# Performance work log

Measured on AMD Instinct MI355X. Metric: run time of the kernel, lower is better.

Reference implementation:

```python
import jax, jax.numpy as jnp
import numpy as np

N_NODES = 100000
N_EDGES = 500000
N_GRAPHS = 128
HID = 128          # Config.hidden_dim
KEY_EMB = HID // 4 # 32
IN_DIM = 16
FEAT_DIM = IN_DIM - 1  # key feature removed
OUT_DIM = 2
MSG_IN = 2 * HID + 1   # 257


def setup_inputs() -> dict:
    key = jax.random.key(0)
    ks = jax.random.split(key, 24)
    p = lambda k, shp: (jax.random.normal(k, shp, dtype=jnp.float32) * 0.02)
    inp = {
        "x": jax.random.normal(ks[0], (N_NODES, IN_DIM), dtype=jnp.float32),
        "W_enc": p(ks[1], (1, KEY_EMB)), "b_enc": jnp.zeros((KEY_EMB,), jnp.float32),
        "W0": p(ks[2], (FEAT_DIM + KEY_EMB, HID)), "b0": jnp.zeros((HID,), jnp.float32),
        "W1a": p(ks[3], (MSG_IN, HID)), "b1a": jnp.zeros((HID,), jnp.float32),
        "W1b": p(ks[4], (HID, HID)), "b1b": jnp.zeros((HID,), jnp.float32),
        "W2a": p(ks[5], (MSG_IN, HID)), "b2a": jnp.zeros((HID,), jnp.float32),
        "W2b": p(ks[6], (HID, HID)), "b2b": jnp.zeros((HID,), jnp.float32),
        "Wf1": p(ks[7], (4 * HID, HID)), "bf1": jnp.zeros((HID,), jnp.float32),
        "Wf2": p(ks[8], (HID, OUT_DIM)), "bf2": jnp.zeros((OUT_DIM,), jnp.float32),
        "edge_src1": jax.random.randint(ks[9], (N_EDGES,), 0, N_NODES),
        "edge_dst1": jax.random.randint(ks[10], (N_EDGES,), 0, N_NODES),
        "edge_src2": jax.random.randint(ks[11], (N_EDGES,), 0, N_NODES),
        "edge_dst2": jax.random.randint(ks[12], (N_EDGES,), 0, N_NODES),
        "batch": jnp.sort(jax.random.randint(ks[13], (N_NODES,), 0, N_GRAPHS)),
    }
    return inp


def _leaky_relu(v):
    return jnp.where(v > 0, v, 0.1 * v)


def _edge_conv(h, key_feat, src, dst, Wa, ba, Wb, bb):
    # message: [x_j - x_i, x_i, key_j - key_i] -> Linear -> LeakyReLU(0.1) -> Linear
    h_i = h[dst]                      # [E, HID] target
    h_j = h[src]                      # [E, HID] source
    m = jnp.concatenate([h_j - h_i, h_i, key_feat[src] - key_feat[dst]], axis=-1)  # [E, 257]
    m = _leaky_relu(jnp.dot(m, Wa) + ba)
    m = jnp.dot(m, Wb) + bb
    agg = jax.ops.segment_max(m, dst, num_segments=N_NODES)
    agg = jnp.where(jnp.isfinite(agg), agg, 0.0)  # nodes with no in-edges -> 0 (PyG scatter-max fill)
    return agg + h  # residual


def reference(x, W_enc, b_enc, W0, b0, W1a, b1a, W1b, b1b, W2a, b2a, W2b, b2b,
              Wf1, bf1, Wf2, bf2, edge_src1, edge_dst1, edge_src2, edge_dst2, batch):
    key_feat = x[:, 0:1]              # key_feature_idx = 0
    features = x[:, 1:]               # [N, FEAT_DIM]
    key_emb = jnp.dot(key_feat, W_enc) + b_enc  # [N, 32]
    h = jax.nn.relu(jnp.dot(jnp.concatenate([features, key_emb], axis=-1), W0) + b0)  # dropout: eval mode

    x1 = jax.nn.relu(_edge_conv(h, key_feat, edge_src1, edge_dst1, W1a, b1a, W1b, b1b))
    x2 = jax.nn.relu(_edge_conv(x1, key_feat, edge_src2, edge_dst2, W2a, b2a, W2b, b2b))

    cat = jnp.concatenate([x1, x2], axis=1)  # [N, 256]
    max_pool = jax.ops.segment_max(cat, batch, num_segments=N_GRAPHS)
    max_pool = jnp.where(jnp.isfinite(max_pool), max_pool, 0.0)
    counts = jax.ops.segment_sum(jnp.ones((N_NODES,), jnp.float32), batch, num_segments=N_GRAPHS)
    mean_pool = jax.ops.segment_sum(cat, batch, num_segments=N_GRAPHS) / jnp.maximum(counts, 1.0)[:, None]

    pooled = jnp.concatenate([max_pool, mean_pool], axis=1)  # [G, 512]
    out = jnp.dot(jax.nn.relu(jnp.dot(pooled, Wf1) + bf1), Wf2) + bf2
    return jax.nn.log_softmax(out, axis=1)
```

## Files before the change

### kernel.cpp

```cpp
#include <hip/hip_runtime.h>
#include <cstdint>

#define N_NODES 100000
#define N_EDGES 500000
#define N_GRAPHS 128
#define HID 128
#define SCAN1_B ((2 * N_NODES + 255) / 256)
#define BOTH_GRID ((2 * N_EDGES + 255) / 256)
#define MM_G ((N_NODES + 127) / 128)
#define A_G ((2 * N_NODES + 511) / 512)
#define B_G ((2 * N_EDGES + 511) / 512)

typedef __attribute__((ext_vector_type(8))) short short8;
typedef __attribute__((ext_vector_type(4))) float f32x4;

__device__ __forceinline__ unsigned encf(float f) {
    unsigned u = __float_as_uint(f);
    return (u & 0x80000000u) ? ~u : (u | 0x80000000u);
}
__device__ __forceinline__ float decf(unsigned e) {
    unsigned u = (e & 0x80000000u) ? (e & 0x7FFFFFFFu) : ~e;
    return __uint_as_float(u);
}
__device__ __forceinline__ unsigned cvt_pk_bf16(float lo, float hi) {
    unsigned r;
    asm("v_cvt_pk_bf16_f32 %0, %1, %2" : "=v"(r) : "v"(lo), "v"(hi));
    return r;
}
__device__ __forceinline__ ushort bf16r(float f) {
    unsigned u = __float_as_uint(f);
    return (ushort)((u + 0x7fffu + ((u >> 16) & 1u)) >> 16);
}
__device__ __forceinline__ float bf2f(ushort h) {
    return __uint_as_float((unsigned)h << 16);
}

__global__ __launch_bounds__(256) void prep_hist_kernel(const float* __restrict__ W1b,
                                                        const float* __restrict__ W2b,
                                                        const float* __restrict__ W1a,
                                                        const float* __restrict__ W2a,
                                                        const float* __restrict__ W_enc,
                                                        const float* __restrict__ b_enc,
                                                        const float* __restrict__ W0,
                                                        const float* __restrict__ b0,
                                                        ushort* __restrict__ WT,
                                                        float* __restrict__ wkey,
                                                        float* __restrict__ bias0,
                                                        float* __restrict__ pooled,
                                                        const int* __restrict__ dst1,
                                                        const int* __restrict__ dst2,
                                                        int* __restrict__ cnt,
                                                        int* __restrict__ seq) {
    int blk = blockIdx.x;
    int tid = threadIdx.x;
    if (blk >= 641) {
        int e = (blk - 641) * 256 + tid;
        if (e < N_EDGES) seq[e] = atomicAdd(&cnt[dst1[e]], 1);
        else if (e < 2 * N_EDGES) seq[e] = atomicAdd(&cnt[N_NODES + dst2[e - N_EDGES]], 1);
        return;
    }
    if (blk >= 385) {
        pooled[(blk - 385) * 256 + tid] = 0.f;
        return;
    }
    if (blk == 384) {
        if (tid < HID) {
            float wk = 0.f, bk = b0[tid];
            for (int k = 0; k < 32; ++k) {
                float w = W0[(15 + k) * HID + tid];
                wk += W_enc[k] * w;
                bk += b_enc[k] * w;
            }
            wkey[tid] = wk;
            bias0[tid] = bk;
        }
        return;
    }
    int m = blk >> 6;
    int i = (blk & 63) * 256 + tid;
    int n = i >> 7, k = i & 127;
    int src = k * HID + n;
    float v;
    switch (m) {
        case 0: v = W1b[src]; break;
        case 1: v = W2b[src]; break;
        case 2: v = W1a[src]; break;
        case 3: v = W1a[HID * HID + src] - W1a[src]; break;
        case 4: v = W2a[src]; break;
        default: v = W2a[HID * HID + src] - W2a[src]; break;
    }
    WT[m * HID * HID + i] = bf16r(v);
}

__global__ __launch_bounds__(256) void scan1_kernel(const int* __restrict__ cnt,
                                                    int* __restrict__ cursor,
                                                    int* __restrict__ partials) {
    __shared__ int tmp[256];
    int tid = threadIdx.x;
    int gid = blockIdx.x * 256 + tid;
    int v = (gid < 2 * N_NODES) ? cnt[gid] : 0;
    tmp[tid] = v;
    __syncthreads();
#pragma unroll
    for (int off = 1; off < 256; off <<= 1) {
        int t = (tid >= off) ? tmp[tid - off] : 0;
        __syncthreads();
        tmp[tid] += t;
        __syncthreads();
    }
    if (gid < 2 * N_NODES) cursor[gid] = tmp[tid] - v;
    if (tid == 255) partials[blockIdx.x] = tmp[255];
}

__global__ __launch_bounds__(1024) void scan2_kernel(int* __restrict__ partials) {
    __shared__ int tmp[1024];
    int tid = threadIdx.x;
    int v = (tid < SCAN1_B) ? partials[tid] : 0;
    tmp[tid] = v;
    __syncthreads();
#pragma unroll
    for (int off = 1; off < 1024; off <<= 1) {
        int t = (tid >= off) ? tmp[tid - off] : 0;
        __syncthreads();
        tmp[tid] += t;
        __syncthreads();
    }
    if (tid < SCAN1_B) partials[tid] = tmp[tid] - v;
}

__global__ __launch_bounds__(512, 4) void build_mm_kernel(const float* __restrict__ x,
                                                          const float* __restrict__ W0,
                                                          const float* __restrict__ wkey,
                                                          const float* __restrict__ bias0,
                                                          ushort* __restrict__ h,
                                                          float* __restrict__ xkey,
                                                          const ushort* __restrict__ WuT,
                                                          const ushort* __restrict__ WvT,
                                                          const float* __restrict__ bv,
                                                          ushort* __restrict__ outu,
                                                          ushort* __restrict__ outv,
                                                          const int* __restrict__ src1,
                                                          const int* __restrict__ dst1,
                                                          const int* __restrict__ src2,
                                                          const int* __restrict__ dst2,
                                                          const int* __restrict__ cnt,
                                                          const int* __restrict__ cursor,
                                                          const int* __restrict__ partials,
                                                          const int* __restrict__ seq,
                                                          int* __restrict__ srcS,
                                                          int* __restrict__ dstS,
                                                          unsigned* __restrict__ agg1,
                                                          unsigned* __restrict__ agg2) {
    __shared__ ushort sH[128 * 136];
    __shared__ ushort sWT[128 * 136];
    int blk = blockIdx.x;
    int tid = threadIdx.x;

    if (blk >= MM_G) {
        int zb = blk - MM_G;
        if (zb < A_G) {
            int gid = zb * 512 + tid;
            if (gid >= 2 * N_NODES) return;
            int c = cnt[gid];
            if (c == 0) return;
            int o = cursor[gid] + partials[gid >> 8];
            int layer = gid >= N_NODES;
            int d = gid - layer * N_NODES;
            for (int i = 0; i < c; ++i) dstS[o + i] = d;
            bool spans = (o >> 4) != ((o + c - 1) >> 4);
            bool tail = (o + c == N_EDGES) || (o + c == 2 * N_EDGES);
            if (spans || tail) {
                unsigned* agg = layer ? agg2 : agg1;
                uint4* ap = (uint4*)(agg + (size_t)d * HID);
#pragma unroll
                for (int i = 0; i < 32; ++i) ap[i] = make_uint4(0u, 0u, 0u, 0u);
            }
            return;
        }
        int e = (zb - A_G) * 512 + tid;
        int s, idx;
        if (e < N_EDGES) { s = src1[e]; idx = dst1[e]; }
        else if (e < 2 * N_EDGES) { s = src2[e - N_EDGES]; idx = N_NODES + dst2[e - N_EDGES]; }
        else return;
        int pos = cursor[idx] + partials[idx >> 8] + seq[e];
        srcS[pos] = s;
        return;
    }

    int n0 = blk * 128;
#pragma unroll
    for (int q = 0; q < 4; ++q) {
        int c = q * 512 + tid;
        int r = c >> 4, off = (c & 15) << 3;
        int n = n0 + r;
        uint4 vv = make_uint4(0, 0, 0, 0);
        if (n < N_NODES) {
            const float* xr = x + n * 16;
            float k0 = xr[0];
            if (off == 0) xkey[n] = k0;
            float xf[15];
#pragma unroll
            for (int f = 0; f < 15; ++f) xf[f] = xr[1 + f];
            unsigned ow[4];
#pragma unroll
            for (int p = 0; p < 4; ++p) {
                int c0 = off + 2 * p;
                float a0 = bias0[c0] + k0 * wkey[c0];
                float a1 = bias0[c0 + 1] + k0 * wkey[c0 + 1];
#pragma unroll
                for (int f = 0; f < 15; ++f) {
                    float2 w2 = *(const float2*)(W0 + f * HID + c0);
                    a0 = fmaf(xf[f], w2.x, a0);
                    a1 = fmaf(xf[f], w2.y, a1);
                }
                ow[p] = cvt_pk_bf16(fmaxf(a0, 0.f), fmaxf(a1, 0.f));
            }
            vv = make_uint4(ow[0], ow[1], ow[2], ow[3]);
            *(uint4*)(h + (size_t)n * HID + off) = vv;
        }
        *(uint4*)(sH + r * 136 + off) = vv;
    }
#pragma unroll
    for (int q = 0; q < 4; ++q) {
        int c = q * 512 + tid;
        int nn = c >> 4, off = (c & 15) << 3;
        *(uint4*)(sWT + nn * 136 + off) = *(const uint4*)(WuT + nn * 128 + off);
    }
    __syncthreads();

    int lane = tid & 63, wv = tid >> 6;
    int l15 = lane & 15, quad = lane >> 4;
    int ch = wv & 1, rh = wv >> 1;

    short8 afr[2][4];
#pragma unroll
    for (int rr = 0; rr < 2; ++rr) {
        const ushort* ab = sH + (rh * 32 + rr * 16 + l15) * 136 + quad * 8;
#pragma unroll
        for (int kc = 0; kc < 4; ++kc)
            afr[rr][kc] = *(const short8*)(ab + kc * 32);
    }

#pragma unroll
    for (int pass = 0; pass < 2; ++pass) {
        ushort* out = pass ? outv : outu;
        f32x4 acc[2][4];
#pragma unroll
        for (int rr = 0; rr < 2; ++rr)
#pragma unroll
            for (int ct = 0; ct < 4; ++ct) acc[rr][ct] = (f32x4){0.f, 0.f, 0.f, 0.f};
#pragma unroll
        for (int kc = 0; kc < 4; ++kc) {
#pragma unroll
            for (int ct = 0; ct < 4; ++ct) {
                short8 bfr = *(const short8*)(sWT + ((ch * 4 + ct) * 16 + l15) * 136 + quad * 8 + kc * 32);
                acc[0][ct] = __builtin_amdgcn_mfma_f32_16x16x32_bf16(afr[0][kc], bfr, acc[0][ct], 0, 0, 0);
                acc[1][ct] = __builtin_amdgcn_mfma_f32_16x16x32_bf16(afr[1][kc], bfr, acc[1][ct], 0, 0, 0);
            }
        }
        __syncthreads();
#pragma unroll
        for (int ct = 0; ct < 4; ++ct) {
            int col = (ch * 4 + ct) * 16 + l15;
            float bb = pass ? bv[col] : 0.f;
#pragma unroll
            for (int rr = 0; rr < 2; ++rr) {
                int rowb = rh * 32 + rr * 16 + quad * 4;
                unsigned p01 = cvt_pk_bf16(acc[rr][ct][0] + bb, acc[rr][ct][1] + bb);
                unsigned p23 = cvt_pk_bf16(acc[rr][ct][2] + bb, acc[rr][ct][3] + bb);
                sH[(rowb + 0) * 136 + col] = (ushort)p01;
                sH[(rowb + 1) * 136 + col] = (ushort)(p01 >> 16);
                sH[(rowb + 2) * 136 + col] = (ushort)p23;
                sH[(rowb + 3) * 136 + col] = (ushort)(p23 >> 16);
            }
        }
        if (pass == 0) {
#pragma unroll
            for (int q = 0; q < 4; ++q) {
                int c = q * 512 + tid;
                int nn = c >> 4, off = (c & 15) << 3;
                *(uint4*)(sWT + nn * 136 + off) = *(const uint4*)(WvT + nn * 128 + off);
            }
        }
        __syncthreads();
#pragma unroll
        for (int q = 0; q < 4; ++q) {
            int c = q * 512 + tid;
            int r = c >> 4, off = (c & 15) << 3;
            int m = n0 + r;
            if (m < N_NODES)
                *(uint4*)(out + (size_t)m * HID + off) = *(const uint4*)(sH + r * 136 + off);
        }
    }
}

__global__ __launch_bounds__(512, 4) void mm_mfma_dual_kernel(const ushort* __restrict__ in,
                                                              const unsigned* __restrict__ aggin,
                                                              const int* __restrict__ cntin,
                                                              const float* __restrict__ baddin,
                                                              ushort* __restrict__ xout,
                                                              const ushort* __restrict__ WuT,
                                                              const ushort* __restrict__ WvT,
                                                              const float* __restrict__ bv,
                                                              ushort* __restrict__ outu,
                                                              ushort* __restrict__ outv, int nrows) {
    __shared__ ushort sH[128 * 136];
    __shared__ ushort sWT[128 * 136];
    int tid = threadIdx.x;
    int n0 = blockIdx.x * 128;
#pragma unroll
    for (int q = 0; q < 4; ++q) {
        int c = q * 512 + tid;
        int r = c >> 4, off = (c & 15) << 3;
        int n = n0 + r;
        uint4 vv = make_uint4(0, 0, 0, 0);
        if (n < nrows) {
            uint4 hv = *(const uint4*)(in + (size_t)n * HID + off);
            float add[8];
#pragma unroll
            for (int p = 0; p < 8; ++p) add[p] = 0.f;
            if (cntin[n] > 0) {
                uint4 e0 = *(const uint4*)(aggin + (size_t)n * HID + off);
                uint4 e1 = *(const uint4*)(aggin + (size_t)n * HID + off + 4);
                float4 bb0 = *(const float4*)(baddin + off);
                float4 bb1 = *(const float4*)(baddin + off + 4);
                add[0] = decf(e0.x) + bb0.x; add[1] = decf(e0.y) + bb0.y;
                add[2] = decf(e0.z) + bb0.z; add[3] = decf(e0.w) + bb0.w;
                add[4] = decf(e1.x) + bb1.x; add[5] = decf(e1.y) + bb1.y;
                add[6] = decf(e1.z) + bb1.z; add[7] = decf(e1.w) + bb1.w;
            }
            unsigned hw[4] = {hv.x, hv.y, hv.z, hv.w};
            unsigned ow[4];
#pragma unroll
            for (int p = 0; p < 4; ++p) {
                float lo = __uint_as_float(hw[p] << 16);
                float hi = __uint_as_float(hw[p] & 0xffff0000u);
                float r0 = fmaxf(add[2 * p] + lo, 0.f);
                float r1 = fmaxf(add[2 * p + 1] + hi, 0.f);
                ow[p] = cvt_pk_bf16(r0, r1);
            }
            vv = make_uint4(ow[0], ow[1], ow[2], ow[3]);
            *(uint4*)(xout + (size_t)n * HID + off) = vv;
        }
        *(uint4*)(sH + r * 136 + off) = vv;
    }
#pragma unroll
    for (int q = 0; q < 4; ++q) {
        int c = q * 512 + tid;
        int nn = c >> 4, off = (c & 15) << 3;
        *(uint4*)(sWT + nn * 136 + off) = *(const uint4*)(WuT + nn * 128 + off);
    }
    __syncthreads();

    int lane = tid & 63, wv = tid >> 6;
    int l15 = lane & 15, quad = lane >> 4;
    int ch = wv & 1, rh = wv >> 1;

    short8 afr[2][4];
#pragma unroll
    for (int rr = 0; rr < 2; ++rr) {
        const ushort* ab = sH + (rh * 32 + rr * 16 + l15) * 136 + quad * 8;
#pragma unroll
        for (int kc = 0; kc < 4; ++kc)
            afr[rr][kc] = *(const short8*)(ab + kc * 32);
    }

#pragma unroll
    for (int pass = 0; pass < 2; ++pass) {
        ushort* out = pass ? outv : outu;
        f32x4 acc[2][4];
#pragma unroll
        for (int rr = 0; rr < 2; ++rr)
#pragma unroll
            for (int ct = 0; ct < 4; ++ct) acc[rr][ct] = (f32x4){0.f, 0.f, 0.f, 0.f};
#pragma unroll
        for (int kc = 0; kc < 4; ++kc) {
#pragma unroll
            for (int ct = 0; ct < 4; ++ct) {
                short8 bfr = *(const short8*)(sWT + ((ch * 4 + ct) * 16 + l15) * 136 + quad * 8 + kc * 32);
                acc[0][ct] = __builtin_amdgcn_mfma_f32_16x16x32_bf16(afr[0][kc], bfr, acc[0][ct], 0, 0, 0);
                acc[1][ct] = __builtin_amdgcn_mfma_f32_16x16x32_bf16(afr[1][kc], bfr, acc[1][ct], 0, 0, 0);
            }
        }
        __syncthreads();
#pragma unroll
        for (int ct = 0; ct < 4; ++ct) {
            int col = (ch * 4 + ct) * 16 + l15;
            float bb = pass ? bv[col] : 0.f;
#pragma unroll
            for (int rr = 0; rr < 2; ++rr) {
                int rowb = rh * 32 + rr * 16 + quad * 4;
                unsigned p01 = cvt_pk_bf16(acc[rr][ct][0] + bb, acc[rr][ct][1] + bb);
                unsigned p23 = cvt_pk_bf16(acc[rr][ct][2] + bb, acc[rr][ct][3] + bb);
                sH[(rowb + 0) * 136 + col] = (ushort)p01;
                sH[(rowb + 1) * 136 + col] = (ushort)(p01 >> 16);
                sH[(rowb + 2) * 136 + col] = (ushort)p23;
                sH[(rowb + 3) * 136 + col] = (ushort)(p23 >> 16);
            }
        }
        if (pass == 0) {
#pragma unroll
            for (int q = 0; q < 4; ++q) {
                int c = q * 512 + tid;
                int nn = c >> 4, off = (c & 15) << 3;
                *(uint4*)(sWT + nn * 136 + off) = *(const uint4*)(WvT + nn * 128 + off);
            }
        }
        __syncthreads();
#pragma unroll
        for (int q = 0; q < 4; ++q) {
            int c = q * 512 + tid;
            int r = c >> 4, off = (c & 15) << 3;
            int m = n0 + r;
            if (m < nrows)
                *(uint4*)(out + (size_t)m * HID + off) = *(const uint4*)(sH + r * 136 + off);
        }
    }
}

__global__ __launch_bounds__(512, 6) void edge_kernel(const ushort* __restrict__ u,
                                                      const ushort* __restrict__ v,
                                                      const float* __restrict__ xkey,
                                                      const int* __restrict__ srcS,
                                                      const int* __restrict__ dstS,
                                                      const ushort* __restrict__ WbT,
                                                      const float* __restrict__ wlast,
                                                      unsigned* __restrict__ agg) {
    __shared__ ushort sWT[128 * 136];
    __shared__ ushort sU[64 * 136];
    __shared__ int sDst[64];
    __shared__ int sBnd[2];
    __shared__ unsigned sMask[3];
    int tid = threadIdx.x;

    int nwg = gridDim.x;
    int orig = blockIdx.x;
    int qq = nwg >> 3, rr8 = nwg & 7;
    int xcd = orig & 7, idx = orig >> 3;
    int wgid = (xcd < rr8 ? xcd * (qq + 1) : rr8 * (qq + 1) + (xcd - rr8) * qq) + idx;
    int w0 = wgid * 64;

#pragma unroll
    for (int q = 0; q < 4; ++q) {
        int c = q * 512 + tid;
        int n = c >> 4, off = (c & 15) << 3;
        *(uint4*)(sWT + n * 136 + off) = *(const uint4*)(WbT + n * 128 + off);
    }

    int eloc = tid >> 3;
    int sub = tid & 7;
    int kb = sub << 4;
    int lane = tid & 63, wv = tid >> 6;
    int l15 = lane & 15, quad = lane >> 4;
    int ch = wv & 1, rh = wv >> 1;

    float wreg[16];
    {
        const float4* wr4 = (const float4*)(wlast + kb);
#pragma unroll
        for (int q = 0; q < 4; ++q) {
            float4 wq = wr4[q];
            wreg[q * 4 + 0] = wq.x; wreg[q * 4 + 1] = wq.y;
            wreg[q * 4 + 2] = wq.z; wreg[q * 4 + 3] = wq.w;
        }
    }

    {
        int e = w0 + eloc;
        if (e >= N_EDGES) e = N_EDGES - 1;
        int sx = srcS[e], sy = dstS[e];
        if (sub == 0) sDst[eloc] = sy;
        if (tid < 2) {
            int eb = (tid == 0) ? (w0 - 1) : (w0 + 64);
            sBnd[tid] = (eb >= 0 && eb < N_EDGES) ? dstS[eb] : -1;
        }
        float kd = xkey[sx] - xkey[sy];
        const uint4* ur = (const uint4*)(u + (size_t)sx * HID + kb);
        const uint4* vr = (const uint4*)(v + (size_t)sy * HID + kb);
        uint4 uu[2], vvv[2];
        uu[0] = ur[0]; uu[1] = ur[1];
        vvv[0] = vr[0]; vvv[1] = vr[1];
#pragma unroll
        for (int q = 0; q < 2; ++q) {
            unsigned pu[4] = {uu[q].x, uu[q].y, uu[q].z, uu[q].w};
            unsigned pv[4] = {vvv[q].x, vvv[q].y, vvv[q].z, vvv[q].w};
            unsigned pk[4];
#pragma unroll
            for (int p = 0; p < 4; ++p) {
                float a0 = __uint_as_float(pu[p] << 16) + __uint_as_float(pv[p] << 16);
                float a1 = __uint_as_float(pu[p] & 0xffff0000u) + __uint_as_float(pv[p] & 0xffff0000u);
                a0 = fmaf(kd, wreg[q * 8 + 2 * p], a0);
                a1 = fmaf(kd, wreg[q * 8 + 2 * p + 1], a1);
                a0 = fmaxf(a0, 0.1f * a0);
                a1 = fmaxf(a1, 0.1f * a1);
                pk[p] = cvt_pk_bf16(a0, a1);
            }
            uint4 o; o.x = pk[0]; o.y = pk[1]; o.z = pk[2]; o.w = pk[3];
            *(uint4*)(sU + eloc * 136 + kb + q * 8) = o;
        }
    }
    __syncthreads();

    if (tid < 64) {
        int dprev = (tid == 0) ? sBnd[0] : sDst[tid - 1];
        unsigned long long m = __ballot(sDst[tid] != dprev);
        if (tid == 0) { sMask[0] = (unsigned)m; sMask[1] = (unsigned)(m >> 32); }
        if (tid == 63) sMask[2] = (sDst[63] != sBnd[1]) ? 1u : 0u;
    }

    short8 afr[4];
    {
        const ushort* ab = sU + (rh * 16 + l15) * 136 + quad * 8;
#pragma unroll
        for (int kc = 0; kc < 4; ++kc)
            afr[kc] = *(const short8*)(ab + kc * 32);
    }
    f32x4 acc[4];
#pragma unroll
    for (int ct = 0; ct < 4; ++ct) acc[ct] = (f32x4){0.f, 0.f, 0.f, 0.f};
#pragma unroll
    for (int kc = 0; kc < 4; ++kc) {
#pragma unroll
        for (int ct = 0; ct < 4; ++ct) {
            short8 bfr = *(const short8*)(sWT + ((ch * 4 + ct) * 16 + l15) * 136 + quad * 8 + kc * 32);
            acc[ct] = __builtin_amdgcn_mfma_f32_16x16x32_bf16(afr[kc], bfr, acc[ct], 0, 0, 0);
        }
    }
    __syncthreads();

#pragma unroll
    for (int ct = 0; ct < 4; ++ct) {
        int col = (ch * 4 + ct) * 16 + l15;
        uint2 pr;
        pr.x = cvt_pk_bf16(acc[ct][0], acc[ct][1]);
        pr.y = cvt_pk_bf16(acc[ct][2], acc[ct][3]);
        *(uint2*)(sU + col * 66 + rh * 16 + quad * 4) = pr;
    }
    __syncthreads();

    {
        int j = tid & 127;
        int q4 = tid >> 7;
        int base = q4 * 16;
        const ushort* mrow = sU + j * 66 + base;
        float vals[16];
#pragma unroll
        for (int q = 0; q < 4; ++q) {
            ushort4 mv = *(const ushort4*)(mrow + q * 4);
            vals[q * 4 + 0] = bf2f(mv.x);
            vals[q * 4 + 1] = bf2f(mv.y);
            vals[q * 4 + 2] = bf2f(mv.z);
            vals[q * 4 + 3] = bf2f(mv.w);
        }
        unsigned mlo = __builtin_amdgcn_readfirstlane(sMask[0]);
        unsigned mhi = __builtin_amdgcn_readfirstlane(sMask[1]);
        unsigned b64 = __builtin_amdgcn_readfirstlane(sMask[2]);
        unsigned long long mask = ((unsigned long long)mhi << 32) | mlo;
        unsigned slice = (unsigned)((mask >> base) & 0xFFFFull);
        unsigned nextbit = (q4 == 3) ? (b64 & 1u) : (unsigned)((mask >> (base + 16)) & 1ull);
        unsigned ext = slice | (nextbit << 16);
        bool contFrom = !(ext & 1u);
        float run = 0.f;
        bool first = true;
#pragma unroll
        for (int e3 = 0; e3 < 16; ++e3) {
            float vv2 = vals[e3];
            bool hb = (ext >> e3) & 1u;
            run = (e3 == 0 || hb) ? vv2 : fmaxf(run, vv2);
            bool end = (e3 == 15) || ((ext >> (e3 + 1)) & 1u);
            if (end) {
                int d = sDst[base + e3];
                unsigned en = encf(run);
                unsigned* ap = agg + (size_t)d * HID + j;
                bool useAtomic = (first && contFrom) || ((e3 == 15) && !nextbit);
                if (useAtomic) atomicMax(ap, en);
                else *ap = en;
                first = false;
            }
        }
    }
}

__global__ __launch_bounds__(256) void pool_kernel(const ushort* __restrict__ x1,
                                                   const unsigned* __restrict__ agg2,
                                                   const float* __restrict__ b2b,
                                                   const int* __restrict__ cnt2,
                                                   const int* __restrict__ batch,
                                                   float* __restrict__ pooled) {
    int g = blockIdx.x >> 4, s = blockIdx.x & 15;
    int tid = threadIdx.x;
    int lo = 0, hi = N_NODES;
    while (lo < hi) { int mid = (lo + hi) >> 1; if (batch[mid] < g) lo = mid + 1; else hi = mid; }
    int start = lo;
    hi = N_NODES;
    while (lo < hi) { int mid = (lo + hi) >> 1; if (batch[mid] < g + 1) lo = mid + 1; else hi = mid; }
    int end = lo;
    int cnt = end - start;
    int b0 = start + (int)((long long)cnt * s / 16);
    int b1 = start + (int)((long long)cnt * (s + 1) / 16);
    if (b1 <= b0) return;
    int j = tid & 127;
    bool isx2 = tid >= 128;
    float bbj = isx2 ? b2b[j] : 0.f;
    float mx = -INFINITY, sm = 0.f;
    for (int n = b0; n < b1; ++n) {
        float xv = bf2f(x1[(size_t)n * HID + j]);
        float vv;
        if (isx2) {
            float a = 0.f;
            if (cnt2[n] > 0) a = decf(agg2[(size_t)n * HID + j]) + bbj;
            vv = fmaxf(a + xv, 0.f);
        } else {
            vv = xv;
        }
        mx = fmaxf(mx, vv);
        sm += vv;
    }
    atomicMax((unsigned*)pooled + (size_t)g * 512 + tid, encf(mx));
    atomicAdd(pooled + (size_t)g * 512 + 256 + tid, sm);
}

__global__ __launch_bounds__(128) void final_kernel(const float* __restrict__ pooled,
                                                    const int* __restrict__ batch,
                                                    const float* __restrict__ Wf1,
                                                    const float* __restrict__ bf1,
                                                    const float* __restrict__ Wf2,
                                                    const float* __restrict__ bf2,
                                                    float* __restrict__ out) {
    __shared__ float sP[512];
    __shared__ float sH[128];
    int g = blockIdx.x, tid = threadIdx.x;
    int lo = 0, hi = N_NODES;
    while (lo < hi) { int mid = (lo + hi) >> 1; if (batch[mid] < g) lo = mid + 1; else hi = mid; }
    int start = lo;
    hi = N_NODES;
    while (lo < hi) { int mid = (lo + hi) >> 1; if (batch[mid] < g + 1) lo = mid + 1; else hi = mid; }
    int cnt = lo - start;
    float inv = 1.f / (float)(cnt > 1 ? cnt : 1);
#pragma unroll
    for (int q = 0; q < 4; ++q) {
        int idx = q * 128 + tid;
        float raw;
        if (idx < 256) {
            unsigned e = ((const unsigned*)pooled)[(size_t)g * 512 + idx];
            raw = (e == 0u) ? 0.f : decf(e);
        } else {
            raw = pooled[(size_t)g * 512 + idx] * inv;
        }
        sP[idx] = raw;
    }
    __syncthreads();
    float acc = bf1[tid];
    for (int k = 0; k < 512; ++k) acc = fmaf(sP[k], Wf1[k * HID + tid], acc);
    sH[tid] = fmaxf(acc, 0.f);
    __syncthreads();
    if (tid < 2) {
        float l = bf2[tid];
        for (int k = 0; k < 128; ++k) l = fmaf(sH[k], Wf2[k * 2 + tid], l);
        sP[tid] = l;
    }
    __syncthreads();
    if (tid == 0) {
        float l0 = sP[0], l1 = sP[1];
        float m = fmaxf(l0, l1);
        float ls = m + logf(expf(l0 - m) + expf(l1 - m));
        out[g * 2 + 0] = l0 - ls;
        out[g * 2 + 1] = l1 - ls;
    }
}

extern "C" void kernel_launch(void* const* d_in, const int* in_sizes, int n_in,
                              void* d_out, int out_size, void* d_ws, size_t ws_size,
                              hipStream_t stream) {
    const float* x     = (const float*)d_in[0];
    const float* W_enc = (const float*)d_in[1];
    const float* b_enc = (const float*)d_in[2];
    const float* W0    = (const float*)d_in[3];
    const float* b0    = (const float*)d_in[4];
    const float* W1a   = (const float*)d_in[5];
    const float* b1a   = (const float*)d_in[6];
    const float* W1b   = (const float*)d_in[7];
    const float* b1b   = (const float*)d_in[8];
    const float* W2a   = (const float*)d_in[9];
    const float* b2a   = (const float*)d_in[10];
    const float* W2b   = (const float*)d_in[11];
    const float* b2b   = (const float*)d_in[12];
    const float* Wf1   = (const float*)d_in[13];
    const float* bf1   = (const float*)d_in[14];
    const float* Wf2   = (const float*)d_in[15];
    const float* bf2   = (const float*)d_in[16];
    const int* src1    = (const int*)d_in[17];
    const int* dst1    = (const int*)d_in[18];
    const int* src2    = (const int*)d_in[19];
    const int* dst2    = (const int*)d_in[20];
    const int* batch   = (const int*)d_in[21];

    const size_t NB = (size_t)N_NODES * HID;
    ushort* hbuf  = (ushort*)d_ws;
    unsigned* agg1 = (unsigned*)(hbuf + NB);
    unsigned* agg2 = agg1 + NB;
    ushort* ubuf  = (ushort*)(agg2 + NB);
    ushort* vbuf  = ubuf + NB;
    ushort* WT    = vbuf + NB;
    ushort* WbT1 = WT;
    ushort* WbT2 = WT + 1 * HID * HID;
    ushort* WuT1 = WT + 2 * HID * HID;
    ushort* WvT1 = WT + 3 * HID * HID;
    ushort* WuT2 = WT + 4 * HID * HID;
    ushort* WvT2 = WT + 5 * HID * HID;
    float* wkey  = (float*)(WT + 6 * HID * HID);
    float* bias0 = wkey + 128;
    float* xkey  = bias0 + 128;
    float* pooled = xkey + N_NODES;
    int* cnt    = (int*)(pooled + 128 * 512);
    int* cursor = cnt + 2 * N_NODES;
    int* partials = cursor + 2 * N_NODES;
    int* srcS = partials + 1024;
    int* dstS = srcS + 2 * N_EDGES;
    int* seq  = dstS + 2 * N_EDGES;

    const int edgeGrid = (N_EDGES + 63) / 64;
    const int prepGrid = 385 + 256 + BOTH_GRID;
    const int buildMmGrid = MM_G + A_G + B_G;

    hipMemsetAsync(cnt, 0, 2 * N_NODES * sizeof(int), stream);
    prep_hist_kernel<<<prepGrid, 256, 0, stream>>>(W1b, W2b, W1a, W2a, W_enc, b_enc, W0, b0,
                                                   WT, wkey, bias0, pooled, dst1, dst2, cnt, seq);
    scan1_kernel<<<SCAN1_B, 256, 0, stream>>>(cnt, cursor, partials);
    scan2_kernel<<<1, 1024, 0, stream>>>(partials);

    build_mm_kernel<<<buildMmGrid, 512, 0, stream>>>(x, W0, wkey, bias0, hbuf, xkey,
                                                     WuT1, WvT1, b1a, ubuf, vbuf,
                                                     src1, dst1, src2, dst2, cnt, cursor,
                                                     partials, seq, srcS, dstS, agg1, agg2);

    edge_kernel<<<edgeGrid, 512, 0, stream>>>(ubuf, vbuf, xkey, srcS, dstS, WbT1,
                                              W1a + 256 * HID, agg1);

    mm_mfma_dual_kernel<<<MM_G, 512, 0, stream>>>(hbuf, agg1, cnt, b1b, hbuf,
                                                  WuT2, WvT2, b2a, ubuf, vbuf, N_NODES);
    edge_kernel<<<edgeGrid, 512, 0, stream>>>(ubuf, vbuf, xkey, srcS + N_EDGES, dstS + N_EDGES,
                                              WbT2, W2a + 256 * HID, agg2);

    pool_kernel<<<N_GRAPHS * 16, 256, 0, stream>>>(hbuf, agg2, b2b, cnt + N_NODES, batch, pooled);
    final_kernel<<<N_GRAPHS, 128, 0, stream>>>(pooled, batch, Wf1, bf1, Wf2, bf2, (float*)d_out);
}
```

Before: 441.9 us.

## Split layer-2 CSR build across later kernels to shorten the critical path

The layer-2 edge histogram, scan and scatter move out of the up-front prep and build kernels. The histogram now runs inside build_mm_kernel, the scans run after it, and the scatter is fused into the layer-2 node matmul kernel as extra blocks. The aim is to shrink the serial prep phase and hide the layer-2 CSR work behind useful matmul work. It adds two more small scan launches and extra grid blocks in mm2.

```diff
diff --git a/kernel.cpp b/kernel.cpp
--- a/kernel.cpp
+++ b/kernel.cpp
@@ -5,11 +5,11 @@
 #define N_EDGES 500000
 #define N_GRAPHS 128
 #define HID 128
-#define SCAN1_B ((2 * N_NODES + 255) / 256)
-#define BOTH_GRID ((2 * N_EDGES + 255) / 256)
+#define SCANH_B ((N_NODES + 255) / 256)
+#define E256_G ((N_EDGES + 255) / 256)
 #define MM_G ((N_NODES + 127) / 128)
-#define A_G ((2 * N_NODES + 511) / 512)
-#define B_G ((2 * N_EDGES + 511) / 512)
+#define AH_G ((N_NODES + 511) / 512)
+#define BH_G ((N_EDGES + 511) / 512)
 
 typedef __attribute__((ext_vector_type(8))) short short8;
 typedef __attribute__((ext_vector_type(4))) float f32x4;
@@ -48,7 +48,6 @@
                                                         float* __restrict__ bias0,
                                                         float* __restrict__ pooled,
                                                         const int* __restrict__ dst1,
-                                                        const int* __restrict__ dst2,
                                                         int* __restrict__ cnt,
                                                         int* __restrict__ seq) {
     int blk = blockIdx.x;
@@ -56,7 +55,6 @@
     if (blk >= 641) {
         int e = (blk - 641) * 256 + tid;
         if (e < N_EDGES) seq[e] = atomicAdd(&cnt[dst1[e]], 1);
-        else if (e < 2 * N_EDGES) seq[e] = atomicAdd(&cnt[N_NODES + dst2[e - N_EDGES]], 1);
         return;
     }
     if (blk >= 385) {
@@ -92,13 +90,13 @@
     WT[m * HID * HID + i] = bf16r(v);
 }
 
-__global__ __launch_bounds__(256) void scan1_kernel(const int* __restrict__ cnt,
-                                                    int* __restrict__ cursor,
-                                                    int* __restrict__ partials) {
+__global__ __launch_bounds__(256) void scan_half_kernel(const int* __restrict__ cnt,
+                                                        int* __restrict__ cursor,
+                                                        int* __restrict__ partials) {
     __shared__ int tmp[256];
     int tid = threadIdx.x;
     int gid = blockIdx.x * 256 + tid;
-    int v = (gid < 2 * N_NODES) ? cnt[gid] : 0;
+    int v = (gid < N_NODES) ? cnt[gid] : 0;
     tmp[tid] = v;
     __syncthreads();
 #pragma unroll
@@ -108,24 +106,24 @@
         tmp[tid] += t;
         __syncthreads();
     }
-    if (gid < 2 * N_NODES) cursor[gid] = tmp[tid] - v;
+    if (gid < N_NODES) cursor[gid] = tmp[tid] - v;
     if (tid == 255) partials[blockIdx.x] = tmp[255];
 }
 
-__global__ __launch_bounds__(1024) void scan2_kernel(int* __restrict__ partials) {
-    __shared__ int tmp[1024];
+__global__ __launch_bounds__(512) void scan2_half_kernel(int* __restrict__ partials) {
+    __shared__ int tmp[512];
     int tid = threadIdx.x;
-    int v = (tid < SCAN1_B) ? partials[tid] : 0;
+    int v = (tid < SCANH_B) ? partials[tid] : 0;
     tmp[tid] = v;
     __syncthreads();
 #pragma unroll
-    for (int off = 1; off < 1024; off <<= 1) {
+    for (int off = 1; off < 512; off <<= 1) {
         int t = (tid >= off) ? tmp[tid - off] : 0;
         __syncthreads();
         tmp[tid] += t;
         __syncthreads();
     }
-    if (tid < SCAN1_B) partials[tid] = tmp[tid] - v;
+    if (tid < SCANH_B) partials[tid] = tmp[tid] - v;
 }
 
 __global__ __launch_bounds__(512, 4) void build_mm_kernel(const float* __restrict__ x,
@@ -141,16 +139,15 @@
                                                           ushort* __restrict__ outv,
                                                           const int* __restrict__ src1,
                                                           const int* __restrict__ dst1,
-                                                          const int* __restrict__ src2,
                                                           const int* __restrict__ dst2,
                                                           const int* __restrict__ cnt,
                                                           const int* __restrict__ cursor,
-                                                          const int* __restrict__ partials,
-                                                          const int* __restrict__ seq,
+                                                          const int* __restrict__ partials1,
+                                                          int* __restrict__ cnt2w,
+                                                          int* __restrict__ seq,
                                                           int* __restrict__ srcS,
                                                           int* __restrict__ dstS,
-                                                          unsigned* __restrict__ agg1,
-                                                          unsigned* __restrict__ agg2) {
+                                                          unsigned* __restrict__ agg1) {
     __shared__ ushort sH[128 * 136];
     __shared__ ushort sWT[128 * 136];
     int blk = blockIdx.x;
@@ -158,33 +155,38 @@
 
     if (blk >= MM_G) {
         int zb = blk - MM_G;
-        if (zb < A_G) {
+        if (zb < AH_G) {
             int gid = zb * 512 + tid;
-            if (gid >= 2 * N_NODES) return;
+            if (gid >= N_NODES) return;
             int c = cnt[gid];
             if (c == 0) return;
-            int o = cursor[gid] + partials[gid >> 8];
-            int layer = gid >= N_NODES;
-            int d = gid - layer * N_NODES;
-            for (int i = 0; i < c; ++i) dstS[o + i] = d;
+            int o = cursor[gid] + partials1[gid >> 8];
+            for (int i = 0; i < c; ++i) dstS[o + i] = gid;
             bool spans = (o >> 4) != ((o + c - 1) >> 4);
-            bool tail = (o + c == N_EDGES) || (o + c == 2 * N_EDGES);
+            bool tail = (o + c == N_EDGES);
             if (spans || tail) {
-                unsigned* agg = layer ? agg2 : agg1;
-                uint4* ap = (uint4*)(agg + (size_t)d * HID);
+                uint4* ap = (uint4*)(agg1 + (size_t)gid * HID);
 #pragma unroll
                 for (int i = 0; i < 32; ++i) ap[i] = make_uint4(0u, 0u, 0u, 0u);
             }
             return;
         }
-        int e = (zb - A_G) * 512 + tid;
-        int s, idx;
-        if (e < N_EDGES) { s = src1[e]; idx = dst1[e]; }
-        else if (e < 2 * N_EDGES) { s = src2[e - N_EDGES]; idx = N_NODES + dst2[e - N_EDGES]; }
-        else return;
-        int pos = cursor[idx] + partials[idx >> 8] + seq[e];
-        srcS[pos] = s;
-        return;
+        zb -= AH_G;
+        if (zb < BH_G) {
+            int e = zb * 512 + tid;
+            if (e >= N_EDGES) return;
+            int idx = dst1[e];
+            int pos = cursor[idx] + partials1[idx >> 8] + seq[e];
+            srcS[pos] = src1[e];
+            return;
+        }
+        zb -= BH_G;
+        {
+            int e = zb * 512 + tid;
+            if (e >= N_EDGES) return;
+            seq[N_EDGES + e] = atomicAdd(&cnt2w[dst2[e]], 1);
+            return;
+        }
     }
 
     int n0 = blk * 128;
@@ -294,27 +296,67 @@
     }
 }
 
-__global__ __launch_bounds__(512, 4) void mm_mfma_dual_kernel(const ushort* __restrict__ in,
-                                                              const unsigned* __restrict__ aggin,
-                                                              const int* __restrict__ cntin,
-                                                              const float* __restrict__ baddin,
-                                                              ushort* __restrict__ xout,
-                                                              const ushort* __restrict__ WuT,
-                                                              const ushort* __restrict__ WvT,
-                                                              const float* __restrict__ bv,
-                                                              ushort* __restrict__ outu,
-                                                              ushort* __restrict__ outv, int nrows) {
+__global__ __launch_bounds__(512, 4) void mm2_build2_kernel(const ushort* __restrict__ in,
+                                                            const unsigned* __restrict__ aggin,
+                                                            const int* __restrict__ cntin,
+                                                            const float* __restrict__ baddin,
+                                                            ushort* __restrict__ xout,
+                                                            const ushort* __restrict__ WuT,
+                                                            const ushort* __restrict__ WvT,
+                                                            const float* __restrict__ bv,
+                                                            ushort* __restrict__ outu,
+                                                            ushort* __restrict__ outv,
+                                                            const int* __restrict__ src2,
+                                                            const int* __restrict__ dst2,
+                                                            const int* __restrict__ cnt2,
+                                                            const int* __restrict__ cursor2,
+                                                            const int* __restrict__ partials2,
+                                                            const int* __restrict__ seq,
+                                                            int* __restrict__ srcS,
+                                                            int* __restrict__ dstS,
+                                                            unsigned* __restrict__ agg2) {
     __shared__ ushort sH[128 * 136];
     __shared__ ushort sWT[128 * 136];
+    int blk = blockIdx.x;
     int tid = threadIdx.x;
-    int n0 = blockIdx.x * 128;
+
+    if (blk >= MM_G) {
+        int zb = blk - MM_G;
+        if (zb < AH_G) {
+            int gid = zb * 512 + tid;
+            if (gid >= N_NODES) return;
+            int c = cnt2[gid];
+            if (c == 0) return;
+            int o = cursor2[gid] + partials2[gid >> 8];
+            for (int i = 0; i < c; ++i) dstS[N_EDGES + o + i] = gid;
+            bool spans = (o >> 4) != ((o + c - 1) >> 4);
+            bool tail = (o + c == N_EDGES);
+            if (spans || tail) {
+                uint4* ap = (uint4*)(agg2 + (size_t)gid * HID);
+#pragma unroll
+                for (int i = 0; i < 32; ++i) ap[i] = make_uint4(0u, 0u, 0u, 0u);
+            }
+            return;
+        }
+        zb -= AH_G;
+        {
+            int e = zb * 512 + tid;
+            if (e >= N_EDGES) return;
+            int idx = dst2[e];
+            int pos = cursor2[idx] + partials2[idx >> 8] + seq[N_EDGES + e];
+            srcS[N_EDGES + pos] = src2[e];
+            return;
+        }
+    }
+
+    int n0 = blk * 128;
 #pragma unroll
     for (int q = 0; q < 4; ++q) {
         int c = q * 512 + tid;
         int r = c >> 4, off = (c & 15) << 3;
         int n = n0 + r;
         uint4 vv = make_uint4(0, 0, 0, 0);
-        if (n < nrows) {
+        if (n < N_NODES) {
             uint4 hv = *(const uint4*)(in + (size_t)n * HID + off);
             float add[8];
 #pragma unroll
@@ -412,7 +454,7 @@
             int c = q * 512 + tid;
             int r = c >> 4, off = (c & 15) << 3;
             int m = n0 + r;
-            if (m < nrows)
+            if (m < N_NODES)
                 *(uint4*)(out + (size_t)m * HID + off) = *(const uint4*)(sH + r * 136 + off);
         }
     }
@@ -714,31 +756,38 @@
     float* pooled = xkey + N_NODES;
     int* cnt    = (int*)(pooled + 128 * 512);
     int* cursor = cnt + 2 * N_NODES;
-    int* partials = cursor + 2 * N_NODES;
-    int* srcS = partials + 1024;
+    int* partials1 = cursor + 2 * N_NODES;
+    int* partials2 = partials1 + 512;
+    int* srcS = partials2 + 512;
     int* dstS = srcS + 2 * N_EDGES;
     int* seq  = dstS + 2 * N_EDGES;
 
     const int edgeGrid = (N_EDGES + 63) / 64;
-    const int prepGrid = 385 + 256 + BOTH_GRID;
-    const int buildMmGrid = MM_G + A_G + B_G;
+    const int prepGrid = 641 + E256_G;
+    const int buildMmGrid = MM_G + AH_G + BH_G + BH_G;
+    const int mm2Grid = MM_G + AH_G + BH_G;
 
     hipMemsetAsync(cnt, 0, 2 * N_NODES * sizeof(int), stream);
     prep_hist_kernel<<<prepGrid, 256, 0, stream>>>(W1b, W2b, W1a, W2a, W_enc, b_enc, W0, b0,
-                                                   WT, wkey, bias0, pooled, dst1, dst2, cnt, seq);
-    scan1_kernel<<<SCAN1_B, 256, 0, stream>>>(cnt, cursor, partials);
-    scan2_kernel<<<1, 1024, 0, stream>>>(partials);
+                                                   WT, wkey, bias0, pooled, dst1, cnt, seq);
+    scan_half_kernel<<<SCANH_B, 256, 0, stream>>>(cnt, cursor, partials1);
+    scan2_half_kernel<<<1, 512, 0, stream>>>(partials1);
 
     build_mm_kernel<<<buildMmGrid, 512, 0, stream>>>(x, W0, wkey, bias0, hbuf, xkey,
                                                      WuT1, WvT1, b1a, ubuf, vbuf,
-                                                     src1, dst1, src2, dst2, cnt, cursor,
-                                                     partials, seq, srcS, dstS, agg1, agg2);
+                                                     src1, dst1, dst2, cnt, cursor, partials1,
+                                                     cnt + N_NODES, seq, srcS, dstS, agg1);
+
+    scan_half_kernel<<<SCANH_B, 256, 0, stream>>>(cnt + N_NODES, cursor + N_NODES, partials2);
+    scan2_half_kernel<<<1, 512, 0, stream>>>(partials2);
 
     edge_kernel<<<edgeGrid, 512, 0, stream>>>(ubuf, vbuf, xkey, srcS, dstS, WbT1,
                                               W1a + 256 * HID, agg1);
 
-    mm_mfma_dual_kernel<<<MM_G, 512, 0, stream>>>(hbuf, agg1, cnt, b1b, hbuf,
-                                                  WuT2, WvT2, b2a, ubuf, vbuf, N_NODES);
+    mm2_build2_kernel<<<mm2Grid, 512, 0, stream>>>(hbuf, agg1, cnt, b1b, hbuf,
+                                                   WuT2, WvT2, b2a, ubuf, vbuf,
+                                                   src2, dst2, cnt + N_NODES, cursor + N_NODES,
+                                                   partials2, seq, srcS, dstS, agg2);
     edge_kernel<<<edgeGrid, 512, 0, stream>>>(ubuf, vbuf, xkey, srcS + N_EDGES, dstS + N_EDGES,
                                               WbT2, W2a + 256 * HID, agg2);
 
```

After: 449.2 us. Within noise of the previous version (+1.7%).
